# Kernel tuning notes

Measured on AMD Instinct MI355X. Metric: run time of the kernel, lower is better.

The kernel has to match this reference:

```python
import jax, jax.numpy as jnp
import numpy as np

N_PATCH = 80
N_FFT = 160
PAD = N_FFT // 2 - N_PATCH // 2  # 40
D = 64       # n_delays
NC = 512     # candidate TFs
L = 0.0064   # physical patch size (m)
DX = 4e-05   # pixel size (m)
FWHM = 0.0015


def setup_inputs() -> dict:
    key = jax.random.key(0)
    k0, k1 = jax.random.split(key)
    patch_stack = jax.random.normal(k0, (1, D, N_PATCH, N_PATCH), jnp.float32)
    # Fourier coordinates (centered grid), as in get_fourier_coord(N=160, l=0.0064)
    f = np.fft.fftshift(np.fft.fftfreq(N_FFT, d=L / N_FFT)) * 2 * np.pi
    KX, KY = np.meshgrid(f, f, indexing='xy')
    k_rad = np.sqrt(KX ** 2 + KY ** 2)
    k2D = jnp.asarray(k_rad, jnp.float32)
    theta2D = jnp.asarray(np.arctan2(KY, KX), jnp.float32)
    # self.k: ifftshifted radial wavenumber, broadcast shape [1,1,160,160]
    k_loss = jnp.asarray(np.fft.ifftshift(k_rad), jnp.float32)[None, None]
    # Gaussian apodization window, sigma = fwhm/4e-5/sqrt(2 ln 2)
    sigma = FWHM / DX / np.sqrt(2.0 * np.log(2.0))
    c = np.arange(N_PATCH) - (N_PATCH - 1) / 2.0
    gx, gy = np.meshgrid(c, c)
    gaussian_window = jnp.asarray(
        np.exp(-(gx ** 2 + gy ** 2) / (2.0 * sigma ** 2)), jnp.float32)[None]
    delays = jnp.linspace(-5e-5, 5e-5, D).astype(jnp.float32)
    # candidate (dc, x, y) wavefront parameters
    cand_params = (jax.random.uniform(k1, (NC, 3), jnp.float32, -1.0, 1.0)
                   * jnp.array([1e-5, 5e-6, 5e-6], jnp.float32))
    return dict(patch_stack=patch_stack, gaussian_window=gaussian_window,
                delays=delays, k2D=k2D, theta2D=theta2D, k_loss=k_loss,
                cand_params=cand_params)


def reference(patch_stack, gaussian_window, delays, k2D, theta2D, k_loss, cand_params):
    n = patch_stack.shape[-1]
    pad = n // 2
    # window, zero-pad to double size, ifftshift, FFT2 -> Y [1, D, 2n, 2n]
    yw = patch_stack * gaussian_window
    ypad = jnp.pad(yw, ((0, 0), (0, 0), (pad, pad), (pad, pad)))
    Y = jnp.fft.fft2(jnp.fft.ifftshift(ypad, axes=(-2, -1)))
    Yabs_k = jnp.abs(Y) * k_loss

    def make_tf(p):
        dc, x, y = p[0], p[1], p[2]
        w = dc + x * jnp.cos(2.0 * theta2D) + y * jnp.sin(2.0 * theta2D)
        # (exp(-i k d) + exp(i k d)) / 2 == cos(k d)  (real-valued TF)
        phase = k2D[None] * (delays[:, None, None] - w[None])  # [D, 2n, 2n]
        return jnp.fft.ifftshift(jnp.cos(phase), axes=(-2, -1))[None]  # [1, D, 2n, 2n]

    def step(carry, p):
        best_loss, best_X, best_idx, idx = carry
        H = make_tf(p)
        rhs = jnp.sum(Y * H, axis=-3, keepdims=True)   # conj(H) == H (real)
        lhs = jnp.sum(H * H, axis=-3, keepdims=True)   # |H|^2
        X = rhs / lhs                                   # [1, 1, 2n, 2n] complex
        loss = jnp.mean((Yabs_k - jnp.abs(H * X) * k_loss) ** 2,
                        axis=(-3, -2, -1))[0]
        better = loss < best_loss
        carry = (jnp.where(better, loss, best_loss),
                 jnp.where(better, X, best_X),
                 jnp.where(better, idx, best_idx),
                 idx + 1)
        return carry, None

    init = (jnp.array(jnp.inf, jnp.float32),
            jnp.zeros((1, 1, 2 * n, 2 * n), jnp.complex64),
            jnp.array(0, jnp.int32), jnp.array(0, jnp.int32))
    (best_loss, best_X, best_idx, _), _ = jax.lax.scan(step, init, cand_params)

    img = jnp.fft.fftshift(jnp.fft.ifft2(best_X), axes=(-2, -1))
    best_x = jnp.real(img[..., pad:pad + n, pad:pad + n])  # crop_half
    best_params = cand_params[best_idx]
    return best_x, best_params, best_loss
```

## Files before the change

kernel.cpp:

```cpp
#include <hip/hip_runtime.h>

#define NF 160
#define NP 80
#define ND 64
#define NC 512
#define NV 81
#define NPIXH (NF*NV)
#define NPIXP 13056
#define NSTR 1632
#define STRIPE 8
#define RECQ 21
#define BT 128
#define CPT 4
#define TWO_PI 6.283185307179586f

#define IP_AR 0
#define IP_AI 1
#define IP_BR 2
#define IP_BI 3
#define IP_P  4
#define IP_Q  5
#define IP_R  6
#define IP_C2T 7
#define IP_S2T 8
#define IP_K  9
#define NPRM 10

__device__ __forceinline__ void rot(float& c, float& s, float stc, float sts) {
  float t1 = s * sts;
  float t2 = s * stc;
  float cn = fmaf(c, stc, -t1);
  s = fmaf(c, sts, t2);
  c = cn;
}

__device__ __forceinline__ void start_i_pow(int n, float& c, float& s) {
  switch (n & 3) {
    case 0: c = 1.f; s = 0.f; break;
    case 1: c = 0.f; s = 1.f; break;
    case 2: c = -1.f; s = 0.f; break;
    default: c = 0.f; s = -1.f; break;
  }
}

__global__ __launch_bounds__(256) void k_fft_x(const float* __restrict__ patch,
                                               const float* __restrict__ gw,
                                               float2* __restrict__ T) {
  int idx = blockIdx.x * 256 + threadIdx.x;
  int v = idx % NV;
  int a = (idx / NV) % NP;
  int d = idx / (NV * NP);
  float c, s;
  start_i_pow(v, c, s);
  float stc, sts;
  sincosf(-TWO_PI * (float)v / (float)NF, &sts, &stc);
  const float* prow = patch + (size_t)(d * NP + a) * NP;
  const float* grow = gw + a * NP;
  float accR = 0.f, accI = 0.f;
#pragma unroll 4
  for (int b = 0; b < NP; ++b) {
    float f = prow[b] * grow[b];
    accR = fmaf(f, c, accR);
    accI = fmaf(f, s, accI);
    rot(c, s, stc, sts);
  }
  T[idx] = make_float2(accR, accI);
}

__global__ __launch_bounds__(256) void k_fft_y(const float2* __restrict__ T,
                                               float2* __restrict__ Y) {
  int idx = blockIdx.x * 256 + threadIdx.x;
  int v = idx % NV;
  int ug = (idx / NV) % 40;
  int d = idx / (NV * 40);
  float c[4], s[4], aR[4], aI[4], stc[4], sts[4];
#pragma unroll
  for (int j = 0; j < 4; ++j) {
    int u = ug * 4 + j;
    start_i_pow(u, c[j], s[j]);
    sincosf(-TWO_PI * (float)u / (float)NF, &sts[j], &stc[j]);
    aR[j] = 0.f; aI[j] = 0.f;
  }
  const float2* Tb = T + (size_t)(d * NP) * NV + v;
#pragma unroll 4
  for (int a = 0; a < NP; ++a) {
    float2 t = Tb[(size_t)a * NV];
#pragma unroll
    for (int j = 0; j < 4; ++j) {
      aR[j] = fmaf(t.x, c[j], aR[j]);
      aR[j] = fmaf(-t.y, s[j], aR[j]);
      aI[j] = fmaf(t.x, s[j], aI[j]);
      aI[j] = fmaf(t.y, c[j], aI[j]);
      rot(c[j], s[j], stc[j], sts[j]);
    }
  }
#pragma unroll
  for (int j = 0; j < 4; ++j) {
    int u = ug * 4 + j;
    Y[((size_t)d * NF + u) * NV + v] = make_float2(aR[j], aI[j]);
  }
}

__global__ __launch_bounds__(256) void k_prep(const float2* __restrict__ Y,
                                              const float* __restrict__ delays,
                                              const float* __restrict__ kloss,
                                              const float* __restrict__ theta,
                                              float4* __restrict__ rec4,
                                              float* __restrict__ prm) {
  __shared__ float ykl[32][65];
  __shared__ float mom[8][32][9];
  int t = threadIdx.x;
  int dg = t >> 5;
  int pl = t & 31;
  int p = blockIdx.x * 32 + pl;
  bool valid = p < NPIXH;
  float k = 0.f, c2t = 0.f, s2t = 0.f, wgt = 0.f;
  int u = 0, v = 0;
  if (valid) {
    u = p / NV; v = p - u * NV;
    k = kloss[u * NF + v];
    float th = theta[((u + 80) % NF) * NF + ((v + 80) % NF)];
    c2t = cosf(2.f * th); s2t = sinf(2.f * th);
    if (v == 0 || v == 80) {
      if (u == 0 || u == 80) wgt = 1.f;
      else if (u < 80) wgt = 2.f;
      else wgt = 0.f;
    } else wgt = 2.f;
  }
  float mAr = 0.f, mAi = 0.f, mBr = 0.f, mBi = 0.f;
  float mP = 0.f, mQ = 0.f, mR = 0.f, mS = 0.f;
#pragma unroll
  for (int j = 0; j < 8; ++j) {
    int d = dg * 8 + j;
    float sd, cd;
    sincosf(k * delays[d], &sd, &cd);
    float yx = 0.f, yy = 0.f;
    if (valid) {
      float2 y = Y[((size_t)d * NF + u) * NV + v];
      yx = y.x; yy = y.y;
    }
    mAr = fmaf(yx, cd, mAr);  mAi = fmaf(yy, cd, mAi);
    mBr = fmaf(yx, sd, mBr);  mBi = fmaf(yy, sd, mBi);
    mP = fmaf(cd, cd, mP);  mQ = fmaf(cd, sd, mQ);  mR = fmaf(sd, sd, mR);
    float yk = sqrtf(fmaf(yx, yx, yy * yy)) * k;
    ykl[pl][d] = yk;
    mS = fmaf(yk, yk, mS);
  }
  mom[dg][pl][0] = mAr; mom[dg][pl][1] = mAi;
  mom[dg][pl][2] = mBr; mom[dg][pl][3] = mBi;
  mom[dg][pl][4] = mP;  mom[dg][pl][5] = mQ;
  mom[dg][pl][6] = mR;  mom[dg][pl][7] = mS;
  __syncthreads();
  {
    int pl2 = t >> 3, val = t & 7;
    float s = 0.f;
#pragma unroll
    for (int g2 = 0; g2 < 8; ++g2) s += mom[g2][pl2][val];
    mom[0][pl2][val] = s;
  }
  __syncthreads();
  {
    int pl3 = t >> 3, q2 = t & 7;
    int p3 = blockIdx.x * 32 + pl3;
#pragma unroll
    for (int h = 0; h < 2; ++h) {
      int jj = q2 * 2 + h;
      float4 q = make_float4(ykl[pl3][2 * jj], ykl[pl3][63 - 2 * jj],
                             ykl[pl3][2 * jj + 1], ykl[pl3][62 - 2 * jj]);
      rec4[(size_t)jj * NPIXP + p3] = q;
    }
  }
  if (dg == 0) {
    float Ar = mom[0][pl][0], Ai = mom[0][pl][1];
    float Br = mom[0][pl][2], Bi = mom[0][pl][3];
    float Pm = mom[0][pl][4], Qm = mom[0][pl][5];
    float Rm = mom[0][pl][6], S0 = mom[0][pl][7];
    if (valid) {
      float d0 = delays[0], d1 = delays[1];
      float sd0f, cd0f, sd1f, cd1f;
      sincosf(k * d0, &sd0f, &cd0f);
      sincosf(k * d1, &sd1f, &cd1f);
      float tcd = 2.f * cosf(k * (d1 - d0));
      rec4[(size_t)16 * NPIXP + p] = make_float4(Ar, Ai, Br, Bi);
      rec4[(size_t)17 * NPIXP + p] = make_float4(Pm, Qm, Rm, S0);
      rec4[(size_t)18 * NPIXP + p] = make_float4(c2t, s2t, k, wgt);
      rec4[(size_t)19 * NPIXP + p] = make_float4(cd0f, sd0f, cd1f, sd1f);
      rec4[(size_t)20 * NPIXP + p] = make_float4(tcd, 0.f, 0.f, 0.f);
      prm[IP_AR * NPIXP + p] = Ar;   prm[IP_AI * NPIXP + p] = Ai;
      prm[IP_BR * NPIXP + p] = Br;   prm[IP_BI * NPIXP + p] = Bi;
      prm[IP_P * NPIXP + p] = Pm;    prm[IP_Q * NPIXP + p] = Qm;
      prm[IP_R * NPIXP + p] = Rm;    prm[IP_C2T * NPIXP + p] = c2t;
      prm[IP_S2T * NPIXP + p] = s2t; prm[IP_K * NPIXP + p] = k;
    } else {
      rec4[(size_t)16 * NPIXP + p] = make_float4(0.f, 0.f, 0.f, 0.f);
      rec4[(size_t)17 * NPIXP + p] = make_float4(1.f, 0.f, 1.f, 0.f);
      rec4[(size_t)18 * NPIXP + p] = make_float4(0.f, 0.f, 0.f, 0.f);
      rec4[(size_t)19 * NPIXP + p] = make_float4(1.f, 0.f, 1.f, 0.f);
      rec4[(size_t)20 * NPIXP + p] = make_float4(2.f, 0.f, 0.f, 0.f);
    }
  }
}

__global__ __launch_bounds__(BT) void k_cand(const float4* __restrict__ rec4,
                                             const float* __restrict__ cand,
                                             float* __restrict__ partial) {
  __shared__ float4 buf[STRIPE][RECQ];
  int t = threadIdx.x;
  int p0 = blockIdx.x * STRIPE;
  float dc[CPT], xx[CPT], yy[CPT], acc[CPT];
#pragma unroll
  for (int ci = 0; ci < CPT; ++ci) {
    int c = t + ci * BT;
    dc[ci] = cand[c * 3 + 0];
    xx[ci] = cand[c * 3 + 1];
    yy[ci] = cand[c * 3 + 2];
    acc[ci] = 0.f;
  }
  for (int q = t; q < STRIPE * RECQ; q += BT) {
    int px = q / RECQ, qq = q - px * RECQ;
    buf[px][qq] = rec4[(size_t)qq * NPIXP + (p0 + px)];
  }
  __syncthreads();
#pragma unroll
  for (int i = 0; i < STRIPE; ++i) {
    const float4* r = &buf[i][0];
    float4 pA = r[16];
    float4 pB = r[17];
    float4 pC = r[18];
    float4 pD = r[19];
    float tcd = r[20].x;
    float4 y0 = r[0];
    float A0[CPT], A1[CPT], B0[CPT], B1[CPT], M[CPT], F0[CPT], F1[CPT];
#pragma unroll
    for (int ci = 0; ci < CPT; ++ci) {
      float w_ = fmaf(xx[ci], pC.x, fmaf(yy[ci], pC.y, dc[ci]));
      float sw, cw;
      __sincosf(pC.z * w_, &sw, &cw);
      float rr = fmaf(cw, pA.x, sw * pA.z);
      float ri = fmaf(cw, pA.y, sw * pA.w);
      float lhs = fmaf(cw * cw, pB.x, fmaf(2.f * cw * sw, pB.y, sw * sw * pB.z));
      float rabs = __builtin_amdgcn_sqrtf(fmaf(rr, rr, ri * ri));
      float rl = __builtin_amdgcn_rcpf(lhs);
      float e = fmaf(-lhs, rl, 1.f);
      rl = fmaf(rl, e, rl);
      float kX = pC.z * rabs * rl;
      F0[ci] = fmaf(kX * kX, lhs, pB.w);
      F1[ci] = -2.f * kX;
      float t0 = pD.x * cw, u0 = pD.y * sw;
      float t1 = pD.z * cw, u1 = pD.w * sw;
      A0[ci] = t0 + u0;  B0[ci] = t0 - u0;
      A1[ci] = t1 + u1;  B1[ci] = t1 - u1;
      float m = y0.x * fabsf(A0[ci]);
      m = fmaf(y0.y, fabsf(B0[ci]), m);
      m = fmaf(y0.z, fabsf(A1[ci]), m);
      m = fmaf(y0.w, fabsf(B1[ci]), m);
      M[ci] = m;
    }
    float4 ykn = r[1];
#pragma unroll
    for (int jj = 1; jj < 16; ++jj) {
      float4 yk = ykn;
      if (jj < 15) ykn = r[jj + 1];
#pragma unroll
      for (int ci = 0; ci < CPT; ++ci) {
        float An = fmaf(tcd, A1[ci], -A0[ci]);
        float Bn = fmaf(tcd, B1[ci], -B0[ci]);
        float m = fmaf(yk.x, fabsf(An), M[ci]);
        m = fmaf(yk.y, fabsf(Bn), m);
        float An2 = fmaf(tcd, An, -A1[ci]);
        float Bn2 = fmaf(tcd, Bn, -B1[ci]);
        m = fmaf(yk.z, fabsf(An2), m);
        m = fmaf(yk.w, fabsf(Bn2), m);
        M[ci] = m;
        A0[ci] = An; A1[ci] = An2;
        B0[ci] = Bn; B1[ci] = Bn2;
      }
    }
#pragma unroll
    for (int ci = 0; ci < CPT; ++ci)
      acc[ci] = fmaf(fmaf(F1[ci], M[ci], F0[ci]), pC.w, acc[ci]);
  }
#pragma unroll
  for (int ci = 0; ci < CPT; ++ci)
    partial[(size_t)blockIdx.x * NC + t + ci * BT] = acc[ci];
}

__global__ __launch_bounds__(256) void k_sum(const float* __restrict__ partial,
                                             float* __restrict__ loss) {
  __shared__ float red[256];
  int c = blockIdx.x;
  float s = 0.f;
  for (int j = threadIdx.x; j < NSTR; j += 256)
    s += partial[(size_t)j * NC + c];
  red[threadIdx.x] = s;
  __syncthreads();
  for (int off = 128; off > 0; off >>= 1) {
    if (threadIdx.x < off) red[threadIdx.x] += red[threadIdx.x + off];
    __syncthreads();
  }
  if (threadIdx.x == 0) loss[c] = red[0];
}

__global__ __launch_bounds__(256) void k_amin_ifftu(const float* __restrict__ loss,
                                                    const float* __restrict__ prm,
                                                    const float* __restrict__ cand,
                                                    float* __restrict__ out,
                                                    float2* __restrict__ G) {
  __shared__ float sl[256];
  __shared__ int si[256];
  __shared__ float xr[NF], xi[NF];
  int c1 = threadIdx.x, c2 = threadIdx.x + 256;
  float s1 = loss[c1], s2 = loss[c2];
  float l; int i;
  if (s2 < s1) { l = s2; i = c2; } else { l = s1; i = c1; }
  sl[threadIdx.x] = l; si[threadIdx.x] = i;
  __syncthreads();
  for (int off = 128; off > 0; off >>= 1) {
    if (threadIdx.x < off) {
      float l2 = sl[threadIdx.x + off]; int i2 = si[threadIdx.x + off];
      if (l2 < sl[threadIdx.x] || (l2 == sl[threadIdx.x] && i2 < si[threadIdx.x])) {
        sl[threadIdx.x] = l2; si[threadIdx.x] = i2;
      }
    }
    __syncthreads();
  }
  int bi = si[0];
  if (blockIdx.x == 0 && threadIdx.x == 0) {
    out[6400] = cand[bi * 3 + 0];
    out[6401] = cand[bi * 3 + 1];
    out[6402] = cand[bi * 3 + 2];
    out[6403] = sl[0] * (1.f / 1638400.f);
  }
  int u = blockIdx.x;
  float dc = cand[bi * 3 + 0], xx = cand[bi * 3 + 1], yy = cand[bi * 3 + 2];
  int v = threadIdx.x;
  if (v < NF) {
    float sign = 1.f;
    int ph;
    if (v <= 80) {
      ph = u * NV + v;
    } else {
      int u2 = (NF - u) % NF;
      ph = u2 * NV + (NF - v);
      sign = -1.f;
    }
    float Ar = prm[IP_AR * NPIXP + ph], Ai = prm[IP_AI * NPIXP + ph];
    float Br = prm[IP_BR * NPIXP + ph], Bi = prm[IP_BI * NPIXP + ph];
    float Pm = prm[IP_P * NPIXP + ph], Qm = prm[IP_Q * NPIXP + ph], Rm = prm[IP_R * NPIXP + ph];
    float c2t = prm[IP_C2T * NPIXP + ph], s2t = prm[IP_S2T * NPIXP + ph];
    float k = prm[IP_K * NPIXP + ph];
    float w_ = fmaf(xx, c2t, fmaf(yy, s2t, dc));
    float sw, cw;
    sincosf(k * w_, &sw, &cw);
    float rr = fmaf(cw, Ar, sw * Br);
    float ri = fmaf(cw, Ai, sw * Bi);
    float lhs = fmaf(cw * cw, Pm, fmaf(2.f * cw * sw, Qm, sw * sw * Rm));
    xr[v] = rr / lhs;
    xi[v] = sign * ri / lhs;
  }
  __syncthreads();
  int b = threadIdx.x;
  if (b < NP) {
    int xb = (b + 120) % NF;
    float stc, sts;
    sincosf(TWO_PI * (float)xb / (float)NF, &sts, &stc);
    float c = 1.f, s = 0.f, accR = 0.f, accI = 0.f;
#pragma unroll 4
    for (int vv = 0; vv < NF; ++vv) {
      float xrv = xr[vv], xiv = xi[vv];
      accR = fmaf(xrv, c, accR); accR = fmaf(-xiv, s, accR);
      accI = fmaf(xrv, s, accI); accI = fmaf(xiv, c, accI);
      rot(c, s, stc, sts);
    }
    G[(size_t)u * NP + b] = make_float2(accR, accI);
  }
}

__global__ __launch_bounds__(256) void k_ifft_y(const float2* __restrict__ G,
                                                float* __restrict__ out) {
  __shared__ float red[4][65];
  int t = threadIdx.x;
  int o = t & 63;
  int slc = t >> 6;
  int idx = blockIdx.x * 64 + o;
  int b = idx % NP;
  int a = idx / NP;
  int ya = (a + 120) % NF;
  float stc, sts;
  sincosf(TWO_PI * (float)ya / (float)NF, &sts, &stc);
  float c, s;
  start_i_pow(ya * slc, c, s);
  float accR = 0.f;
  const float2* Gb = G + (size_t)(slc * 40) * NP + b;
#pragma unroll 4
  for (int j = 0; j < 40; ++j) {
    float2 g = Gb[(size_t)j * NP];
    accR = fmaf(g.x, c, accR);
    accR = fmaf(-g.y, s, accR);
    rot(c, s, stc, sts);
  }
  red[slc][o] = accR;
  __syncthreads();
  if (t < 64) {
    float s4 = ((red[0][t] + red[1][t]) + (red[2][t] + red[3][t]));
    out[blockIdx.x * 64 + t] = s4 * (1.f / 25600.f);
  }
}

extern "C" void kernel_launch(void* const* d_in, const int* in_sizes, int n_in,
                              void* d_out, int out_size, void* d_ws, size_t ws_size,
                              hipStream_t stream) {
  (void)in_sizes; (void)n_in; (void)out_size; (void)ws_size;
  const float* patch  = (const float*)d_in[0];
  const float* gw     = (const float*)d_in[1];
  const float* delays = (const float*)d_in[2];
  const float* theta  = (const float*)d_in[4];
  const float* kloss  = (const float*)d_in[5];
  const float* cand   = (const float*)d_in[6];
  float* out = (float*)d_out;

  char* ws = (char*)d_ws;
  size_t off = 0;
  float2* Y = (float2*)(ws + off);      off += (size_t)ND * NF * NV * 8;
  float2* T = (float2*)(ws + off);      off += (size_t)ND * NP * NV * 8;
  float4* rec4 = (float4*)(ws + off);   off += (size_t)RECQ * NPIXP * 16;
  float* prm = (float*)(ws + off);      off += (size_t)NPRM * NPIXP * 4;
  float* partial = (float*)(ws + off);  off += (size_t)NSTR * NC * 4;
  float* loss = (float*)(ws + off);     off += (size_t)NC * 4;
  float2* G = (float2*)(ws + off);      off += (size_t)NF * NP * 8;

  hipLaunchKernelGGL(k_fft_x, dim3((ND * NP * NV) / 256), dim3(256), 0, stream, patch, gw, T);
  hipLaunchKernelGGL(k_fft_y, dim3((ND * 40 * NV) / 256), dim3(256), 0, stream, T, Y);
  hipLaunchKernelGGL(k_prep, dim3(408), dim3(256), 0, stream, Y, delays, kloss, theta, rec4, prm);
  hipLaunchKernelGGL(k_cand, dim3(NSTR), dim3(BT), 0, stream, rec4, cand, partial);
  hipLaunchKernelGGL(k_sum, dim3(NC), dim3(256), 0, stream, partial, loss);
  hipLaunchKernelGGL(k_amin_ifftu, dim3(NF), dim3(256), 0, stream, loss, prm, cand, out, G);
  hipLaunchKernelGGL(k_ifft_y, dim3(100), dim3(256), 0, stream, G, out);
}
```

Measured before the change: 94.72 us.

## Fuse per-pixel moment prep into candidate kernel, drop rec4 buffer

The separate k_prep kernel is removed. Each k_cand block now computes the delay-moments and |Y|·k records for its own 8 pixels directly into shared memory, using 16 lanes per pixel and shuffle reductions. This saves one kernel launch and the global write and read of the rec4 intermediate. In exchange, every candidate block does extra transcendental and reduction work before its main loop, and the reduction now runs in wavefront shuffles.

```diff
diff --git a/kernel.cpp b/kernel.cpp
--- a/kernel.cpp
+++ b/kernel.cpp
@@ -101,112 +101,96 @@
   }
 }
 
-__global__ __launch_bounds__(256) void k_prep(const float2* __restrict__ Y,
-                                              const float* __restrict__ delays,
-                                              const float* __restrict__ kloss,
-                                              const float* __restrict__ theta,
-                                              float4* __restrict__ rec4,
-                                              float* __restrict__ prm) {
-  __shared__ float ykl[32][65];
-  __shared__ float mom[8][32][9];
-  int t = threadIdx.x;
-  int dg = t >> 5;
-  int pl = t & 31;
-  int p = blockIdx.x * 32 + pl;
-  bool valid = p < NPIXH;
-  float k = 0.f, c2t = 0.f, s2t = 0.f, wgt = 0.f;
-  int u = 0, v = 0;
-  if (valid) {
-    u = p / NV; v = p - u * NV;
-    k = kloss[u * NF + v];
-    float th = theta[((u + 80) % NF) * NF + ((v + 80) % NF)];
-    c2t = cosf(2.f * th); s2t = sinf(2.f * th);
-    if (v == 0 || v == 80) {
-      if (u == 0 || u == 80) wgt = 1.f;
-      else if (u < 80) wgt = 2.f;
-      else wgt = 0.f;
-    } else wgt = 2.f;
-  }
-  float mAr = 0.f, mAi = 0.f, mBr = 0.f, mBi = 0.f;
-  float mP = 0.f, mQ = 0.f, mR = 0.f, mS = 0.f;
-#pragma unroll
-  for (int j = 0; j < 8; ++j) {
-    int d = dg * 8 + j;
-    float sd, cd;
-    sincosf(k * delays[d], &sd, &cd);
-    float yx = 0.f, yy = 0.f;
-    if (valid) {
-      float2 y = Y[((size_t)d * NF + u) * NV + v];
-      yx = y.x; yy = y.y;
-    }
-    mAr = fmaf(yx, cd, mAr);  mAi = fmaf(yy, cd, mAi);
-    mBr = fmaf(yx, sd, mBr);  mBi = fmaf(yy, sd, mBi);
-    mP = fmaf(cd, cd, mP);  mQ = fmaf(cd, sd, mQ);  mR = fmaf(sd, sd, mR);
-    float yk = sqrtf(fmaf(yx, yx, yy * yy)) * k;
-    ykl[pl][d] = yk;
-    mS = fmaf(yk, yk, mS);
-  }
-  mom[dg][pl][0] = mAr; mom[dg][pl][1] = mAi;
-  mom[dg][pl][2] = mBr; mom[dg][pl][3] = mBi;
-  mom[dg][pl][4] = mP;  mom[dg][pl][5] = mQ;
-  mom[dg][pl][6] = mR;  mom[dg][pl][7] = mS;
-  __syncthreads();
-  {
-    int pl2 = t >> 3, val = t & 7;
-    float s = 0.f;
-#pragma unroll
-    for (int g2 = 0; g2 < 8; ++g2) s += mom[g2][pl2][val];
-    mom[0][pl2][val] = s;
-  }
-  __syncthreads();
-  {
-    int pl3 = t >> 3, q2 = t & 7;
-    int p3 = blockIdx.x * 32 + pl3;
-#pragma unroll
-    for (int h = 0; h < 2; ++h) {
-      int jj = q2 * 2 + h;
-      float4 q = make_float4(ykl[pl3][2 * jj], ykl[pl3][63 - 2 * jj],
-                             ykl[pl3][2 * jj + 1], ykl[pl3][62 - 2 * jj]);
-      rec4[(size_t)jj * NPIXP + p3] = q;
-    }
-  }
-  if (dg == 0) {
-    float Ar = mom[0][pl][0], Ai = mom[0][pl][1];
-    float Br = mom[0][pl][2], Bi = mom[0][pl][3];
-    float Pm = mom[0][pl][4], Qm = mom[0][pl][5];
-    float Rm = mom[0][pl][6], S0 = mom[0][pl][7];
-    if (valid) {
-      float d0 = delays[0], d1 = delays[1];
-      float sd0f, cd0f, sd1f, cd1f;
-      sincosf(k * d0, &sd0f, &cd0f);
-      sincosf(k * d1, &sd1f, &cd1f);
-      float tcd = 2.f * cosf(k * (d1 - d0));
-      rec4[(size_t)16 * NPIXP + p] = make_float4(Ar, Ai, Br, Bi);
-      rec4[(size_t)17 * NPIXP + p] = make_float4(Pm, Qm, Rm, S0);
-      rec4[(size_t)18 * NPIXP + p] = make_float4(c2t, s2t, k, wgt);
-      rec4[(size_t)19 * NPIXP + p] = make_float4(cd0f, sd0f, cd1f, sd1f);
-      rec4[(size_t)20 * NPIXP + p] = make_float4(tcd, 0.f, 0.f, 0.f);
-      prm[IP_AR * NPIXP + p] = Ar;   prm[IP_AI * NPIXP + p] = Ai;
-      prm[IP_BR * NPIXP + p] = Br;   prm[IP_BI * NPIXP + p] = Bi;
-      prm[IP_P * NPIXP + p] = Pm;    prm[IP_Q * NPIXP + p] = Qm;
-      prm[IP_R * NPIXP + p] = Rm;    prm[IP_C2T * NPIXP + p] = c2t;
-      prm[IP_S2T * NPIXP + p] = s2t; prm[IP_K * NPIXP + p] = k;
-    } else {
-      rec4[(size_t)16 * NPIXP + p] = make_float4(0.f, 0.f, 0.f, 0.f);
-      rec4[(size_t)17 * NPIXP + p] = make_float4(1.f, 0.f, 1.f, 0.f);
-      rec4[(size_t)18 * NPIXP + p] = make_float4(0.f, 0.f, 0.f, 0.f);
-      rec4[(size_t)19 * NPIXP + p] = make_float4(1.f, 0.f, 1.f, 0.f);
-      rec4[(size_t)20 * NPIXP + p] = make_float4(2.f, 0.f, 0.f, 0.f);
-    }
-  }
-}
-
-__global__ __launch_bounds__(BT) void k_cand(const float4* __restrict__ rec4,
+__global__ __launch_bounds__(BT) void k_cand(const float2* __restrict__ Y,
+                                             const float* __restrict__ delays,
+                                             const float* __restrict__ kloss,
+                                             const float* __restrict__ theta,
                                              const float* __restrict__ cand,
-                                             float* __restrict__ partial) {
+                                             float* __restrict__ partial,
+                                             float* __restrict__ prm) {
   __shared__ float4 buf[STRIPE][RECQ];
+  __shared__ float ykl[STRIPE][65];
   int t = threadIdx.x;
   int p0 = blockIdx.x * STRIPE;
+
+  {
+    int px = t >> 4;
+    int dg = t & 15;
+    int p = p0 + px;
+    bool valid = p < NPIXH;
+    float k = 0.f, c2t = 0.f, s2t = 0.f, wgt = 0.f;
+    int u = 0, v = 0;
+    if (valid) {
+      u = p / NV; v = p - u * NV;
+      k = kloss[u * NF + v];
+      float th = theta[((u + 80) % NF) * NF + ((v + 80) % NF)];
+      c2t = cosf(2.f * th); s2t = sinf(2.f * th);
+      if (v == 0 || v == 80) {
+        if (u == 0 || u == 80) wgt = 1.f;
+        else if (u < 80) wgt = 2.f;
+        else wgt = 0.f;
+      } else wgt = 2.f;
+    }
+    float mAr = 0.f, mAi = 0.f, mBr = 0.f, mBi = 0.f;
+    float mP = 0.f, mQ = 0.f, mR = 0.f, mS = 0.f;
+    float cd0t = 1.f, sd0t = 0.f, cd1t = 1.f, sd1t = 0.f;
+#pragma unroll
+    for (int j = 0; j < 4; ++j) {
+      int d = dg * 4 + j;
+      float sd, cd;
+      sincosf(k * delays[d], &sd, &cd);
+      float yx = 0.f, yy = 0.f;
+      if (valid) {
+        float2 y = Y[((size_t)d * NF + u) * NV + v];
+        yx = y.x; yy = y.y;
+      }
+      mAr = fmaf(yx, cd, mAr);  mAi = fmaf(yy, cd, mAi);
+      mBr = fmaf(yx, sd, mBr);  mBi = fmaf(yy, sd, mBi);
+      mP = fmaf(cd, cd, mP);  mQ = fmaf(cd, sd, mQ);  mR = fmaf(sd, sd, mR);
+      float yk = sqrtf(fmaf(yx, yx, yy * yy)) * k;
+      ykl[px][d] = yk;
+      mS = fmaf(yk, yk, mS);
+      if (j == 0) { cd0t = cd; sd0t = sd; }
+      if (j == 1) { cd1t = cd; sd1t = sd; }
+    }
+#pragma unroll
+    for (int off = 8; off > 0; off >>= 1) {
+      mAr += __shfl_xor(mAr, off);
+      mAi += __shfl_xor(mAi, off);
+      mBr += __shfl_xor(mBr, off);
+      mBi += __shfl_xor(mBi, off);
+      mP += __shfl_xor(mP, off);
+      mQ += __shfl_xor(mQ, off);
+      mR += __shfl_xor(mR, off);
+      mS += __shfl_xor(mS, off);
+    }
+    if (dg == 0) {
+      if (valid) {
+        float tcd = 2.f * cosf(k * (delays[1] - delays[0]));
+        buf[px][16] = make_float4(mAr, mAi, mBr, mBi);
+        buf[px][17] = make_float4(mP, mQ, mR, mS);
+        buf[px][18] = make_float4(c2t, s2t, k, wgt);
+        buf[px][19] = make_float4(cd0t, sd0t, cd1t, sd1t);
+        buf[px][20] = make_float4(tcd, 0.f, 0.f, 0.f);
+        prm[IP_AR * NPIXP + p] = mAr;  prm[IP_AI * NPIXP + p] = mAi;
+        prm[IP_BR * NPIXP + p] = mBr;  prm[IP_BI * NPIXP + p] = mBi;
+        prm[IP_P * NPIXP + p] = mP;    prm[IP_Q * NPIXP + p] = mQ;
+        prm[IP_R * NPIXP + p] = mR;    prm[IP_C2T * NPIXP + p] = c2t;
+        prm[IP_S2T * NPIXP + p] = s2t; prm[IP_K * NPIXP + p] = k;
+      } else {
+        buf[px][16] = make_float4(0.f, 0.f, 0.f, 0.f);
+        buf[px][17] = make_float4(1.f, 0.f, 1.f, 0.f);
+        buf[px][18] = make_float4(0.f, 0.f, 0.f, 0.f);
+        buf[px][19] = make_float4(1.f, 0.f, 1.f, 0.f);
+        buf[px][20] = make_float4(2.f, 0.f, 0.f, 0.f);
+      }
+    }
+    int px2 = t >> 4, jj = t & 15;
+    buf[px2][jj] = make_float4(ykl[px2][2 * jj], ykl[px2][63 - 2 * jj],
+                               ykl[px2][2 * jj + 1], ykl[px2][62 - 2 * jj]);
+  }
+  __syncthreads();
+
   float dc[CPT], xx[CPT], yy[CPT], acc[CPT];
 #pragma unroll
   for (int ci = 0; ci < CPT; ++ci) {
@@ -216,11 +200,6 @@
     yy[ci] = cand[c * 3 + 2];
     acc[ci] = 0.f;
   }
-  for (int q = t; q < STRIPE * RECQ; q += BT) {
-    int px = q / RECQ, qq = q - px * RECQ;
-    buf[px][qq] = rec4[(size_t)qq * NPIXP + (p0 + px)];
-  }
-  __syncthreads();
 #pragma unroll
   for (int i = 0; i < STRIPE; ++i) {
     const float4* r = &buf[i][0];
@@ -423,7 +402,6 @@
   size_t off = 0;
   float2* Y = (float2*)(ws + off);      off += (size_t)ND * NF * NV * 8;
   float2* T = (float2*)(ws + off);      off += (size_t)ND * NP * NV * 8;
-  float4* rec4 = (float4*)(ws + off);   off += (size_t)RECQ * NPIXP * 16;
   float* prm = (float*)(ws + off);      off += (size_t)NPRM * NPIXP * 4;
   float* partial = (float*)(ws + off);  off += (size_t)NSTR * NC * 4;
   float* loss = (float*)(ws + off);     off += (size_t)NC * 4;
@@ -431,8 +409,7 @@
 
   hipLaunchKernelGGL(k_fft_x, dim3((ND * NP * NV) / 256), dim3(256), 0, stream, patch, gw, T);
   hipLaunchKernelGGL(k_fft_y, dim3((ND * 40 * NV) / 256), dim3(256), 0, stream, T, Y);
-  hipLaunchKernelGGL(k_prep, dim3(408), dim3(256), 0, stream, Y, delays, kloss, theta, rec4, prm);
-  hipLaunchKernelGGL(k_cand, dim3(NSTR), dim3(BT), 0, stream, rec4, cand, partial);
+  hipLaunchKernelGGL(k_cand, dim3(NSTR), dim3(BT), 0, stream, Y, delays, kloss, theta, cand, partial, prm);
   hipLaunchKernelGGL(k_sum, dim3(NC), dim3(256), 0, stream, partial, loss);
   hipLaunchKernelGGL(k_amin_ifftu, dim3(NF), dim3(256), 0, stream, loss, prm, cand, out, G);
   hipLaunchKernelGGL(k_ifft_y, dim3(100), dim3(256), 0, stream, G, out);
```

Result: faster. 90.28 us (-4.7%).
